# Kernel optimization log

Measured on AMD Instinct MI355X. Metric: run time of the kernel, lower is better.

The kernel has to match this reference:

```python
import jax, jax.numpy as jnp
import numpy as np

RES_H, RES_W = 64, 64
INV_SMOOTHNESS = 0.1
OFFSET = 0.5
LOSS_WEIGHT = 1.0


def bilinear_sample(mask, xs, ys):
    # mask: [IH, IW]; xs: [Wo]; ys: [Ho] in pixel coords -> [Ho, Wo]
    IH, IW = mask.shape
    x0 = jnp.floor(xs); y0 = jnp.floor(ys)
    wx = xs - x0; wy = ys - y0
    x0i = jnp.clip(x0.astype(jnp.int32), 0, IW - 1)
    x1i = jnp.clip(x0i + 1, 0, IW - 1)
    y0i = jnp.clip(y0.astype(jnp.int32), 0, IH - 1)
    y1i = jnp.clip(y0i + 1, 0, IH - 1)
    g = lambda yi, xi: mask[yi[:, None], xi[None, :]]
    return ((1 - wy)[:, None] * ((1 - wx)[None, :] * g(y0i, x0i) + wx[None, :] * g(y0i, x1i))
            + wy[:, None] * ((1 - wx)[None, :] * g(y1i, x0i) + wx[None, :] * g(y1i, x1i)))


def crop_and_resize(masks, boxes, Ho, Wo):
    # masks: [N, IH, IW]; boxes: [N, 4] xyxy -> binarized [N, Ho, Wo]
    def one(mask, box):
        x1, y1, x2, y2 = box[0], box[1], box[2], box[3]
        xs = x1 + (x2 - x1) * (jnp.arange(Wo, dtype=masks.dtype) + 0.5) / Wo - 0.5
        ys = y1 + (y2 - y1) * (jnp.arange(Ho, dtype=masks.dtype) + 0.5) / Ho - 0.5
        return bilinear_sample(mask, xs, ys)
    out = jax.vmap(one)(masks, boxes)
    return (out >= 0.5).astype(masks.dtype)


def rasterize_mask(verts, H, W, inv_s):
    # Soft polygon rasterization, MODE_MASK: sigmoid(sign * min_sq_dist * inv_s).
    # verts: [N, V, 2] (x, y) in pixel coords of the HxW grid.
    N, V, _ = verts.shape
    xs = jnp.arange(W, dtype=verts.dtype)
    ys = jnp.arange(H, dtype=verts.dtype)
    px = jnp.tile(xs, H)       # [P] with P = H*W
    py = jnp.repeat(ys, W)     # [P]
    p = jnp.stack([px, py], -1)  # [P, 2]
    a = verts                          # [N, V, 2]
    b = jnp.roll(verts, -1, axis=1)    # next vertex (closed polygon)
    ab = b - a                         # [N, V, 2]
    denom = jnp.sum(ab * ab, -1)       # [N, V]
    pa = p[None, :, None, :] - a[:, None, :, :]            # [N, P, V, 2]
    t = jnp.clip(jnp.einsum('npvc,nvc->npv', pa, ab) / (denom[:, None, :] + 1e-12), 0.0, 1.0)
    diff = pa - t[..., None] * ab[:, None, :, :]
    d2 = jnp.sum(diff * diff, -1)      # [N, P, V] squared point-to-segment dist
    d2min = jnp.min(d2, -1)            # [N, P]
    # even-odd crossing test for inside/outside sign
    ay = a[..., 1][:, None, :]; by = b[..., 1][:, None, :]     # [N, 1, V]
    pyb = py[None, :, None]
    cond = (ay > pyb) != (by > pyb)                             # [N, P, V]
    dy = ab[..., 1][:, None, :]
    safe_dy = jnp.where(dy == 0, 1.0, dy)
    xint = a[..., 0][:, None, :] + (pyb - ay) * ab[..., 0][:, None, :] / safe_dy
    crossings = jnp.sum((cond & (px[None, :, None] < xint)).astype(jnp.int32), -1)  # [N, P]
    sign = jnp.where(crossings % 2 == 1, 1.0, -1.0)
    return jax.nn.sigmoid(sign * d2min * inv_s).reshape(N, H, W)


def dice_loss(inp, tgt):
    n = inp.shape[0]
    smooth = 1.0
    iflat = inp.reshape(n, -1)
    tflat = tgt.reshape(n, -1)
    inter = jnp.sum(iflat * tflat, -1)
    losses = 1.0 - (2.0 * inter + smooth) / (jnp.sum(iflat, -1) + jnp.sum(tflat, -1) + smooth)
    return jnp.sum(losses) / n


def setup_inputs() -> dict:
    key = jax.random.key(0)
    k1, k2, k3, k4, k5, k6 = jax.random.split(key, 6)
    N, V, IMG = 128, 128, 512
    # star-shaped polygons (realistic contours) in image coords
    ctr = jax.random.uniform(k1, (N, 1, 2)) * (IMG * 0.6) + IMG * 0.2
    ang = jnp.linspace(0.0, 2.0 * jnp.pi, V, endpoint=False)
    rad = 20.0 + jax.random.uniform(k2, (N, V)) * 60.0
    preds = ctr + jnp.stack([rad * jnp.cos(ang), rad * jnp.sin(ang)], -1)  # [N, V, 2]
    # gt boxes xyxy
    x1y1 = jax.random.uniform(k3, (N, 2)) * (IMG * 0.3)
    wh = 50.0 + jax.random.uniform(k4, (N, 2)) * (IMG * 0.4)
    targets_bboxes = jnp.concatenate([x1y1, x1y1 + wh], -1)  # [N, 4]
    # gt full-image masks: random disks
    cb = jax.random.uniform(k5, (N, 2)) * IMG
    r = 30.0 + jax.random.uniform(k6, (N,)) * 100.0
    yy = jnp.arange(IMG, dtype=jnp.float32)[None, :, None]
    xx = jnp.arange(IMG, dtype=jnp.float32)[None, None, :]
    targets_masks = (((xx - cb[:, 0, None, None]) ** 2 + (yy - cb[:, 1, None, None]) ** 2)
                     < (r[:, None, None] ** 2)).astype(jnp.float32)  # [N, IMG, IMG]
    return {"preds": preds, "targets_masks": targets_masks, "targets_bboxes": targets_bboxes}


def reference(preds, targets_masks, targets_bboxes):
    # union bboxes of predicted polygon extent and gt bbox
    pmin = jnp.min(preds, axis=1)
    pmax = jnp.max(preds, axis=1)
    ub = jnp.concatenate([jnp.minimum(pmin, targets_bboxes[:, :2]),
                          jnp.maximum(pmax, targets_bboxes[:, 2:4])], -1)  # [N, 4]
    # crop + resize + binarize gt masks at the union boxes
    tgt = crop_and_resize(targets_masks, ub, RES_H, RES_W)  # [N, 64, 64]
    # normalize polygons into the (detached) union box
    ubd = jax.lax.stop_gradient(ub)
    normed = (preds - ubd[:, None, :2]) / (ubd[:, None, 2:4] - ubd[:, None, :2])
    verts = normed * float(RES_W) - OFFSET
    pred_masks = rasterize_mask(verts, RES_H, RES_W, INV_SMOOTHNESS)  # [N, 64, 64]
    pred_masks = jnp.clip(pred_masks, 1e-5, 0.99999)
    return dice_loss(pred_masks, tgt) * LOSS_WEIGHT
```

## Files before the change

### kernel.cpp

```cpp
#include <hip/hip_runtime.h>
#include <hip/hip_bf16.h>

#define NMASK 128
#define NV    128
#define IMG   512
#define RES   64
#define PB    8
#define NBLK  (NMASK*PB)
#define BT    256

#define EDGES_OFF 0
#define UB_OFF    131072
#define ACC_OFF   131584
#define FLAG_OFF  131968

#define CULL_D2 118.0f

__device__ __forceinline__ int clampi(int v, int lo, int hi) {
    return v < lo ? lo : (v > hi ? hi : v);
}

__device__ __forceinline__ int detect_bf16(const void* preds) {
    const __hip_bfloat16* pb = (const __hip_bfloat16*)preds;
    int lane = threadIdx.x & 63;
    float v = __bfloat162float(pb[2 * lane]);
    bool ok = (v >= 1.0f) && (v <= 600.0f);
    unsigned long long m = __ballot(ok);
    return (m == 0xFFFFFFFFFFFFFFFFULL) ? 1 : 0;
}

__device__ __forceinline__ float loadf(const void* p, long idx, int isb) {
    if (isb) return __bfloat162float(((const __hip_bfloat16*)p)[idx]);
    return ((const float*)p)[idx];
}

__global__ void __launch_bounds__(128) setup_kernel(
    const void* __restrict__ preds,
    const void* __restrict__ bboxes,
    float* __restrict__ ws)
{
    int n = blockIdx.x, t = threadIdx.x;
    int isb = detect_bf16(preds);

    float vx = loadf(preds, ((long)n*NV + t)*2 + 0, isb);
    float vy = loadf(preds, ((long)n*NV + t)*2 + 1, isb);

    float mnx = vx, mxx = vx, mny = vy, mxy = vy;
    for (int off = 32; off >= 1; off >>= 1) {
        mnx = fminf(mnx, __shfl_xor(mnx, off));
        mxx = fmaxf(mxx, __shfl_xor(mxx, off));
        mny = fminf(mny, __shfl_xor(mny, off));
        mxy = fmaxf(mxy, __shfl_xor(mxy, off));
    }
    __shared__ float r[2][4];
    int w = t >> 6;
    if ((t & 63) == 0) { r[w][0]=mnx; r[w][1]=mxx; r[w][2]=mny; r[w][3]=mxy; }
    __syncthreads();
    mnx = fminf(r[0][0], r[1][0]);
    mxx = fmaxf(r[0][1], r[1][1]);
    mny = fminf(r[0][2], r[1][2]);
    mxy = fmaxf(r[0][3], r[1][3]);

    float bx1 = loadf(bboxes, n*4 + 0, isb);
    float by1 = loadf(bboxes, n*4 + 1, isb);
    float bx2 = loadf(bboxes, n*4 + 2, isb);
    float by2 = loadf(bboxes, n*4 + 3, isb);
    float ux1 = fminf(mnx, bx1), uy1 = fminf(mny, by1);
    float ux2 = fmaxf(mxx, bx2), uy2 = fmaxf(mxy, by2);
    float sx = (float)RES / (ux2 - ux1);
    float sy = (float)RES / (uy2 - uy1);

    __shared__ float2 vn[NV];
    vn[t] = make_float2((vx - ux1)*sx - 0.5f, (vy - uy1)*sy - 0.5f);
    __syncthreads();

    float2 a = vn[t];
    float2 b = vn[(t + 1) & (NV - 1)];
    float abx = b.x - a.x, aby = b.y - a.y;
    float inv = 1.0f / (abx*abx + aby*aby + 1e-12f);
    float slope = abx / ((aby == 0.0f) ? 1.0f : aby);

    float4* eg = (float4*)(ws + EDGES_OFF + (size_t)n * NV * 8);
    eg[2*t]   = make_float4(a.x, a.y, abx, aby);
    eg[2*t+1] = make_float4(abx*inv, aby*inv, slope, b.y);

    if (t == 0) {
        ws[UB_OFF + n*4 + 0] = ux1;
        ws[UB_OFF + n*4 + 1] = uy1;
        ws[UB_OFF + n*4 + 2] = ux2;
        ws[UB_OFF + n*4 + 3] = uy2;
        ws[ACC_OFF + n*3 + 0] = 0.0f;
        ws[ACC_OFF + n*3 + 1] = 0.0f;
        ws[ACC_OFF + n*3 + 2] = 0.0f;
        if (n == 0) ((int*)ws)[FLAG_OFF] = isb;
    }
}

__global__ void __launch_bounds__(BT) MaskRasterizationLoss_2705829396671_kernel(
    const void* __restrict__ masks,
    const float4* __restrict__ edges,
    const float* __restrict__ meta,
    float* __restrict__ acc)
{
    int n    = blockIdx.x >> 3;
    int part = blockIdx.x & 7;
    int t    = threadIdx.x;
    int lane = t & 63;

    const float4* eg = edges + (size_t)n * NV * 2;

    float ux1 = meta[UB_OFF + n*4 + 0], uy1 = meta[UB_OFF + n*4 + 1];
    float ux2 = meta[UB_OFF + n*4 + 2], uy2 = meta[UB_OFF + n*4 + 3];
    int isb = ((const int*)meta)[FLAG_OFF];

    int p0 = part * 512 + t * 2;
    float py  = (float)(p0 >> 6);
    float pxb = (float)(p0 & 63);
    float px1v = pxb + 1.0f;

    float Ylo = (float)(part * 8);
    float Yhi = (float)(part * 8 + 7);

    __shared__ float4 sNA[NV];
    __shared__ float2 sNB[NV];
    __shared__ float4 sCR[NV];
    __shared__ int cnts[2];
    if (t < 2) cnts[t] = 0;
    __syncthreads();

    {
        int e = t & (NV - 1);
        float4 eA = eg[2*e];
        float4 eB = eg[2*e+1];
        if (t < 128) {
            float bxv = eA.x + eA.z;
            float xmn = fminf(eA.x, bxv), xmx = fmaxf(eA.x, bxv);
            float ymn = fminf(eA.y, eB.w), ymx = fmaxf(eA.y, eB.w);
            float dx = fmaxf(fmaxf(xmn - 63.0f, -xmx), 0.0f);
            float dy = fmaxf(fmaxf(ymn - Yhi, Ylo - ymx), 0.0f);
            float lb = fmaf(dx, dx, dy*dy);
            bool keep = lb < CULL_D2;
            unsigned long long m = __ballot(keep);
            int pre = __popcll(m & ((1ull << lane) - 1ull));
            int base = 0;
            if (lane == 0) base = atomicAdd(&cnts[0], (int)__popcll(m));
            base = __shfl(base, 0);
            if (keep) {
                int p = base + pre;
                sNA[p] = eA;
                sNB[p] = make_float2(eB.x, eB.y);
            }
        } else {
            float ymn = fminf(eA.y, eB.w), ymx = fmaxf(eA.y, eB.w);
            bool keep = !((ymn > Yhi) || (ymx <= Ylo));
            unsigned long long m = __ballot(keep);
            int pre = __popcll(m & ((1ull << lane) - 1ull));
            int base = 0;
            if (lane == 0) base = atomicAdd(&cnts[1], (int)__popcll(m));
            base = __shfl(base, 0);
            if (keep) {
                int p = base + pre;
                sCR[p] = make_float4(eA.x, eA.y, eB.z, eB.w);
            }
        }
    }
    __syncthreads();
    int nNear  = __builtin_amdgcn_readfirstlane(cnts[0]);
    int nCross = __builtin_amdgcn_readfirstlane(cnts[1]);

    float d2m0 = 1e30f, d2m1 = 1e30f;
    int   cr0 = 0, cr1 = 0;

    #pragma unroll 4
    for (int i = 0; i < nNear; ++i) {
        float4 A = sNA[i];
        float2 B = sNB[i];

        float pay  = py - A.y;
        float q    = pay * B.y;
        {
            float pax = pxb - A.x;
            float tt  = fmaf(pax, B.x, q);
            tt = fminf(fmaxf(tt, 0.0f), 1.0f);
            float dx  = fmaf(-tt, A.z, pax);
            float dyv = fmaf(-tt, A.w, pay);
            float d2  = fmaf(dx, dx, dyv*dyv);
            d2m0 = fminf(d2m0, d2);
        }
        {
            float pax = px1v - A.x;
            float tt  = fmaf(pax, B.x, q);
            tt = fminf(fmaxf(tt, 0.0f), 1.0f);
            float dx  = fmaf(-tt, A.z, pax);
            float dyv = fmaf(-tt, A.w, pay);
            float d2  = fmaf(dx, dx, dyv*dyv);
            d2m1 = fminf(d2m1, d2);
        }
    }

    #pragma unroll 4
    for (int i = 0; i < nCross; ++i) {
        float4 C = sCR[i];

        float pay  = py - C.y;
        bool  cnd  = (C.y > py) != (C.w > py);
        float xint = fmaf(pay, C.z, C.x);
        cr0 += (cnd && (pxb  < xint)) ? 1 : 0;
        cr1 += (cnd && (px1v < xint)) ? 1 : 0;
    }

    long mbase = (long)n * IMG * IMG;
    float invW = (ux2 - ux1) * (1.0f/(float)RES);
    float invH = (uy2 - uy1) * (1.0f/(float)RES);
    float ys = fmaf(py + 0.5f, invH, uy1) - 0.5f;
    float fy = floorf(ys), wy = ys - fy;
    int y0i = clampi((int)fy, 0, IMG-1);
    int y1i = clampi(y0i + 1, 0, IMG-1);

    float s_pred = 0.0f, s_tgt = 0.0f, s_int = 0.0f;
    #pragma unroll
    for (int k = 0; k < 2; ++k) {
        float px    = k ? px1v : pxb;
        float d2min = k ? d2m1 : d2m0;
        int   cross = k ? cr1  : cr0;

        float sgn = (cross & 1) ? 1.0f : -1.0f;
        float z = sgn * d2min * 0.1f;
        float sg = 1.0f / (1.0f + __expf(-z));
        sg = fminf(fmaxf(sg, 1e-5f), 0.99999f);

        float xs = fmaf(px + 0.5f, invW, ux1) - 0.5f;
        float fx = floorf(xs), wx = xs - fx;
        int x0i = clampi((int)fx, 0, IMG-1);
        int x1i = clampi(x0i + 1, 0, IMG-1);
        float g00 = loadf(masks, mbase + (long)y0i*IMG + x0i, isb);
        float g01 = loadf(masks, mbase + (long)y0i*IMG + x1i, isb);
        float g10 = loadf(masks, mbase + (long)y1i*IMG + x0i, isb);
        float g11 = loadf(masks, mbase + (long)y1i*IMG + x1i, isb);
        float bil = (1.0f-wy) * ((1.0f-wx)*g00 + wx*g01)
                  +        wy * ((1.0f-wx)*g10 + wx*g11);
        float tg = (bil >= 0.5f) ? 1.0f : 0.0f;

        s_pred += sg;
        s_tgt  += tg;
        s_int  += sg * tg;
    }

    for (int off = 32; off >= 1; off >>= 1) {
        s_pred += __shfl_xor(s_pred, off);
        s_tgt  += __shfl_xor(s_tgt,  off);
        s_int  += __shfl_xor(s_int,  off);
    }
    __shared__ float red[3][4];
    int wave = t >> 6;
    if ((t & 63) == 0) { red[0][wave]=s_pred; red[1][wave]=s_tgt; red[2][wave]=s_int; }
    __syncthreads();
    if (t == 0) {
        atomicAdd(&acc[n*3+0], red[0][0]+red[0][1]+red[0][2]+red[0][3]);
        atomicAdd(&acc[n*3+1], red[1][0]+red[1][1]+red[1][2]+red[1][3]);
        atomicAdd(&acc[n*3+2], red[2][0]+red[2][1]+red[2][2]+red[2][3]);
    }
}

__global__ void __launch_bounds__(128) finalize_kernel(
    const float* __restrict__ acc, void* __restrict__ out)
{
    int t = threadIdx.x;
    float sp = acc[t*3+0], st = acc[t*3+1], si = acc[t*3+2];
    float loss = 1.0f - (2.0f*si + 1.0f) / (sp + st + 1.0f);
    for (int off = 32; off >= 1; off >>= 1)
        loss += __shfl_xor(loss, off);
    __shared__ float tmp[2];
    if ((t & 63) == 0) tmp[t >> 6] = loss;
    __syncthreads();
    if (t == 0) {
        float L = (tmp[0] + tmp[1]) * (1.0f/128.0f);
        unsigned int fb = __float_as_uint(L);
        unsigned int r  = (fb + 0x7FFFu + ((fb >> 16) & 1u)) >> 16;
        ((unsigned int*)out)[0] = (r << 16) | r;
    }
}

extern "C" void kernel_launch(void* const* d_in, const int* in_sizes, int n_in,
                              void* d_out, int out_size, void* d_ws, size_t ws_size,
                              hipStream_t stream) {
    const void* preds  = d_in[0];
    const void* masks  = d_in[1];
    const void* bboxes = d_in[2];
    float* ws = (float*)d_ws;

    setup_kernel<<<NMASK, 128, 0, stream>>>(preds, bboxes, ws);
    MaskRasterizationLoss_2705829396671_kernel<<<NBLK, BT, 0, stream>>>(
        masks, (const float4*)(ws + EDGES_OFF), ws, ws + ACC_OFF);
    finalize_kernel<<<1, 128, 0, stream>>>(ws + ACC_OFF, d_out);
}
```

Before: 184.3 us.

## Fuse setup kernel into main raster kernel and replace atomics with per-block partials

Removes the separate setup launch. Each of the 8 blocks per mask now recomputes the union box, the normalized vertices and the edge data directly in shared memory instead of reading them back from global workspace. The global float atomics are replaced by per-block partial sums that the finalize kernel adds up, which also removes the need to zero the accumulators. This saves one kernel launch and a global round trip, at the cost of doing the setup work redundantly in every block.

```diff
diff --git a/kernel.cpp b/kernel.cpp
--- a/kernel.cpp
+++ b/kernel.cpp
@@ -9,10 +9,7 @@
 #define NBLK  (NMASK*PB)
 #define BT    256
 
-#define EDGES_OFF 0
-#define UB_OFF    131072
-#define ACC_OFF   131584
-#define FLAG_OFF  131968
+#define PACC_OFF 0
 
 #define CULL_D2 118.0f
 
@@ -34,32 +31,46 @@
     return ((const float*)p)[idx];
 }
 
-__global__ void __launch_bounds__(128) setup_kernel(
+__global__ void __launch_bounds__(BT) MaskRasterizationLoss_2705829396671_kernel(
     const void* __restrict__ preds,
+    const void* __restrict__ masks,
     const void* __restrict__ bboxes,
-    float* __restrict__ ws)
+    float* __restrict__ pacc)
 {
-    int n = blockIdx.x, t = threadIdx.x;
+    int n    = blockIdx.x >> 3;
+    int part = blockIdx.x & 7;
+    int t    = threadIdx.x;
+    int lane = t & 63;
+
     int isb = detect_bf16(preds);
 
-    float vx = loadf(preds, ((long)n*NV + t)*2 + 0, isb);
-    float vy = loadf(preds, ((long)n*NV + t)*2 + 1, isb);
-
-    float mnx = vx, mxx = vx, mny = vy, mxy = vy;
-    for (int off = 32; off >= 1; off >>= 1) {
-        mnx = fminf(mnx, __shfl_xor(mnx, off));
-        mxx = fmaxf(mxx, __shfl_xor(mxx, off));
-        mny = fminf(mny, __shfl_xor(mny, off));
-        mxy = fmaxf(mxy, __shfl_xor(mxy, off));
-    }
     __shared__ float r[2][4];
-    int w = t >> 6;
-    if ((t & 63) == 0) { r[w][0]=mnx; r[w][1]=mxx; r[w][2]=mny; r[w][3]=mxy; }
-    __syncthreads();
-    mnx = fminf(r[0][0], r[1][0]);
-    mxx = fmaxf(r[0][1], r[1][1]);
-    mny = fminf(r[0][2], r[1][2]);
-    mxy = fmaxf(r[0][3], r[1][3]);
+    __shared__ float2 vn[NV];
+    __shared__ float4 sNA[NV];
+    __shared__ float2 sNB[NV];
+    __shared__ float4 sCR[NV];
+    __shared__ int cnts[2];
+    if (t < 2) cnts[t] = 0;
+
+    float vx = 0.0f, vy = 0.0f;
+    if (t < NV) {
+        vx = loadf(preds, ((long)n*NV + t)*2 + 0, isb);
+        vy = loadf(preds, ((long)n*NV + t)*2 + 1, isb);
+        float mnx = vx, mxx = vx, mny = vy, mxy = vy;
+        for (int off = 32; off >= 1; off >>= 1) {
+            mnx = fminf(mnx, __shfl_xor(mnx, off));
+            mxx = fmaxf(mxx, __shfl_xor(mxx, off));
+            mny = fminf(mny, __shfl_xor(mny, off));
+            mxy = fmaxf(mxy, __shfl_xor(mxy, off));
+        }
+        int w = t >> 6;
+        if (lane == 0) { r[w][0]=mnx; r[w][1]=mxx; r[w][2]=mny; r[w][3]=mxy; }
+    }
+    __syncthreads();
+    float mnx = fminf(r[0][0], r[1][0]);
+    float mxx = fmaxf(r[0][1], r[1][1]);
+    float mny = fminf(r[0][2], r[1][2]);
+    float mxy = fmaxf(r[0][3], r[1][3]);
 
     float bx1 = loadf(bboxes, n*4 + 0, isb);
     float by1 = loadf(bboxes, n*4 + 1, isb);
@@ -70,103 +81,51 @@
     float sx = (float)RES / (ux2 - ux1);
     float sy = (float)RES / (uy2 - uy1);
 
-    __shared__ float2 vn[NV];
-    vn[t] = make_float2((vx - ux1)*sx - 0.5f, (vy - uy1)*sy - 0.5f);
-    __syncthreads();
-
-    float2 a = vn[t];
-    float2 b = vn[(t + 1) & (NV - 1)];
-    float abx = b.x - a.x, aby = b.y - a.y;
-    float inv = 1.0f / (abx*abx + aby*aby + 1e-12f);
-    float slope = abx / ((aby == 0.0f) ? 1.0f : aby);
-
-    float4* eg = (float4*)(ws + EDGES_OFF + (size_t)n * NV * 8);
-    eg[2*t]   = make_float4(a.x, a.y, abx, aby);
-    eg[2*t+1] = make_float4(abx*inv, aby*inv, slope, b.y);
-
-    if (t == 0) {
-        ws[UB_OFF + n*4 + 0] = ux1;
-        ws[UB_OFF + n*4 + 1] = uy1;
-        ws[UB_OFF + n*4 + 2] = ux2;
-        ws[UB_OFF + n*4 + 3] = uy2;
-        ws[ACC_OFF + n*3 + 0] = 0.0f;
-        ws[ACC_OFF + n*3 + 1] = 0.0f;
-        ws[ACC_OFF + n*3 + 2] = 0.0f;
-        if (n == 0) ((int*)ws)[FLAG_OFF] = isb;
-    }
-}
-
-__global__ void __launch_bounds__(BT) MaskRasterizationLoss_2705829396671_kernel(
-    const void* __restrict__ masks,
-    const float4* __restrict__ edges,
-    const float* __restrict__ meta,
-    float* __restrict__ acc)
-{
-    int n    = blockIdx.x >> 3;
-    int part = blockIdx.x & 7;
-    int t    = threadIdx.x;
-    int lane = t & 63;
-
-    const float4* eg = edges + (size_t)n * NV * 2;
-
-    float ux1 = meta[UB_OFF + n*4 + 0], uy1 = meta[UB_OFF + n*4 + 1];
-    float ux2 = meta[UB_OFF + n*4 + 2], uy2 = meta[UB_OFF + n*4 + 3];
-    int isb = ((const int*)meta)[FLAG_OFF];
+    if (t < NV) vn[t] = make_float2((vx - ux1)*sx - 0.5f, (vy - uy1)*sy - 0.5f);
+    __syncthreads();
+
+    float Ylo = (float)(part * 8);
+    float Yhi = (float)(part * 8 + 7);
+
+    if (t < NV) {
+        float2 a = vn[t];
+        float2 b = vn[(t + 1) & (NV - 1)];
+        float abx = b.x - a.x, aby = b.y - a.y;
+        float inv = 1.0f / (abx*abx + aby*aby + 1e-12f);
+        float slope = abx / ((aby == 0.0f) ? 1.0f : aby);
+
+        float xmn = fminf(a.x, b.x), xmx = fmaxf(a.x, b.x);
+        float ymn = fminf(a.y, b.y), ymx = fmaxf(a.y, b.y);
+
+        float dx = fmaxf(fmaxf(xmn - 63.0f, -xmx), 0.0f);
+        float dy = fmaxf(fmaxf(ymn - Yhi, Ylo - ymx), 0.0f);
+        float lb = fmaf(dx, dx, dy*dy);
+        bool keepN = lb < CULL_D2;
+        unsigned long long m = __ballot(keepN);
+        int pre  = __popcll(m & ((1ull << lane) - 1ull));
+        int base = 0;
+        if (lane == 0) base = atomicAdd(&cnts[0], (int)__popcll(m));
+        base = __shfl(base, 0);
+        if (keepN) {
+            sNA[base+pre] = make_float4(a.x, a.y, abx, aby);
+            sNB[base+pre] = make_float2(abx*inv, aby*inv);
+        }
+
+        bool keepC = !((ymn > Yhi) || (ymx <= Ylo));
+        m = __ballot(keepC);
+        pre = __popcll(m & ((1ull << lane) - 1ull));
+        if (lane == 0) base = atomicAdd(&cnts[1], (int)__popcll(m));
+        base = __shfl(base, 0);
+        if (keepC) sCR[base+pre] = make_float4(a.x, a.y, slope, b.y);
+    }
+    __syncthreads();
+    int nNear  = __builtin_amdgcn_readfirstlane(cnts[0]);
+    int nCross = __builtin_amdgcn_readfirstlane(cnts[1]);
 
     int p0 = part * 512 + t * 2;
     float py  = (float)(p0 >> 6);
     float pxb = (float)(p0 & 63);
     float px1v = pxb + 1.0f;
-
-    float Ylo = (float)(part * 8);
-    float Yhi = (float)(part * 8 + 7);
-
-    __shared__ float4 sNA[NV];
-    __shared__ float2 sNB[NV];
-    __shared__ float4 sCR[NV];
-    __shared__ int cnts[2];
-    if (t < 2) cnts[t] = 0;
-    __syncthreads();
-
-    {
-        int e = t & (NV - 1);
-        float4 eA = eg[2*e];
-        float4 eB = eg[2*e+1];
-        if (t < 128) {
-            float bxv = eA.x + eA.z;
-            float xmn = fminf(eA.x, bxv), xmx = fmaxf(eA.x, bxv);
-            float ymn = fminf(eA.y, eB.w), ymx = fmaxf(eA.y, eB.w);
-            float dx = fmaxf(fmaxf(xmn - 63.0f, -xmx), 0.0f);
-            float dy = fmaxf(fmaxf(ymn - Yhi, Ylo - ymx), 0.0f);
-            float lb = fmaf(dx, dx, dy*dy);
-            bool keep = lb < CULL_D2;
-            unsigned long long m = __ballot(keep);
-            int pre = __popcll(m & ((1ull << lane) - 1ull));
-            int base = 0;
-            if (lane == 0) base = atomicAdd(&cnts[0], (int)__popcll(m));
-            base = __shfl(base, 0);
-            if (keep) {
-                int p = base + pre;
-                sNA[p] = eA;
-                sNB[p] = make_float2(eB.x, eB.y);
-            }
-        } else {
-            float ymn = fminf(eA.y, eB.w), ymx = fmaxf(eA.y, eB.w);
-            bool keep = !((ymn > Yhi) || (ymx <= Ylo));
-            unsigned long long m = __ballot(keep);
-            int pre = __popcll(m & ((1ull << lane) - 1ull));
-            int base = 0;
-            if (lane == 0) base = atomicAdd(&cnts[1], (int)__popcll(m));
-            base = __shfl(base, 0);
-            if (keep) {
-                int p = base + pre;
-                sCR[p] = make_float4(eA.x, eA.y, eB.z, eB.w);
-            }
-        }
-    }
-    __syncthreads();
-    int nNear  = __builtin_amdgcn_readfirstlane(cnts[0]);
-    int nCross = __builtin_amdgcn_readfirstlane(cnts[1]);
 
     float d2m0 = 1e30f, d2m1 = 1e30f;
     int   cr0 = 0, cr1 = 0;
@@ -256,17 +215,23 @@
     if ((t & 63) == 0) { red[0][wave]=s_pred; red[1][wave]=s_tgt; red[2][wave]=s_int; }
     __syncthreads();
     if (t == 0) {
-        atomicAdd(&acc[n*3+0], red[0][0]+red[0][1]+red[0][2]+red[0][3]);
-        atomicAdd(&acc[n*3+1], red[1][0]+red[1][1]+red[1][2]+red[1][3]);
-        atomicAdd(&acc[n*3+2], red[2][0]+red[2][1]+red[2][2]+red[2][3]);
+        pacc[blockIdx.x*3+0] = red[0][0]+red[0][1]+red[0][2]+red[0][3];
+        pacc[blockIdx.x*3+1] = red[1][0]+red[1][1]+red[1][2]+red[1][3];
+        pacc[blockIdx.x*3+2] = red[2][0]+red[2][1]+red[2][2]+red[2][3];
     }
 }
 
 __global__ void __launch_bounds__(128) finalize_kernel(
-    const float* __restrict__ acc, void* __restrict__ out)
+    const float* __restrict__ pacc, void* __restrict__ out)
 {
     int t = threadIdx.x;
-    float sp = acc[t*3+0], st = acc[t*3+1], si = acc[t*3+2];
+    float sp = 0.0f, st = 0.0f, si = 0.0f;
+    #pragma unroll
+    for (int p = 0; p < PB; ++p) {
+        sp += pacc[(t*PB + p)*3 + 0];
+        st += pacc[(t*PB + p)*3 + 1];
+        si += pacc[(t*PB + p)*3 + 2];
+    }
     float loss = 1.0f - (2.0f*si + 1.0f) / (sp + st + 1.0f);
     for (int off = 32; off >= 1; off >>= 1)
         loss += __shfl_xor(loss, off);
@@ -289,8 +254,7 @@
     const void* bboxes = d_in[2];
     float* ws = (float*)d_ws;
 
-    setup_kernel<<<NMASK, 128, 0, stream>>>(preds, bboxes, ws);
     MaskRasterizationLoss_2705829396671_kernel<<<NBLK, BT, 0, stream>>>(
-        masks, (const float4*)(ws + EDGES_OFF), ws, ws + ACC_OFF);
-    finalize_kernel<<<1, 128, 0, stream>>>(ws + ACC_OFF, d_out);
-}
+        preds, masks, bboxes, ws + PACC_OFF);
+    finalize_kernel<<<1, 128, 0, stream>>>(ws + PACC_OFF, d_out);
+}
```

After: 181.9 us. About the same (-1.3%).
